# Performance work log

Hardware: AMD Instinct MI355X
Metric: run time of the kernel (lower is better)

Reference implementation:

```python
import jax, jax.numpy as jnp
import numpy as np

N_NODES = 50000
N_EDGES = 800000
IN_DIM = 100
HIDDEN = 16
N_CLASSES = 40


def setup_inputs() -> dict:
    key = jax.random.key(0)
    k1, k2, k3, k4, k5, k6 = jax.random.split(key, 6)
    features = jax.random.normal(k1, (N_NODES, IN_DIM), dtype=jnp.float32)
    edge_src = jax.random.randint(k2, (N_EDGES,), 0, N_NODES, dtype=jnp.int32)
    edge_dst = jax.random.randint(k3, (N_EDGES,), 0, N_NODES, dtype=jnp.int32)
    edge_vals = jax.random.uniform(k4, (N_EDGES,), dtype=jnp.float32)
    W1 = jax.random.uniform(k5, (IN_DIM, HIDDEN), dtype=jnp.float32)
    W2 = jax.random.uniform(k6, (HIDDEN, N_CLASSES), dtype=jnp.float32)
    return {"features": features, "edge_src": edge_src, "edge_dst": edge_dst,
            "edge_vals": edge_vals, "W1": W1, "W2": W2}


def _spmm(edge_src, edge_dst, edge_vals, x):
    # z = A @ x with A given as (dst, src, val) edge list; equivalent to the
    # partition-loop addmm accumulation in broadcast().
    msgs = edge_vals[:, None] * x[edge_src]            # [E, d]
    return jax.ops.segment_sum(msgs, edge_dst, num_segments=x.shape[0])


def reference(features, edge_src, edge_dst, edge_vals, W1, W2):
    h = jax.nn.relu(_spmm(edge_src, edge_dst, edge_vals, features) @ W1)  # [N, 16]
    out = _spmm(edge_src, edge_dst, edge_vals, h) @ W2                    # [N, C]
    return jax.nn.log_softmax(out, axis=1)
```

## Files before the change

kernel.cpp:

```cpp
#include <hip/hip_runtime.h>

#define N_NODES   50000
#define N_EDGES   800000
#define IN_DIM    100
#define HIDDEN    16
#define N_CLASSES 40

#define BSHIFT 6
#define NPB    64
#define NBKT   782
#define PB     256
#define EPB    3125
#define BTW    (NBKT + 1)
#define CAP    2048

#define GROWS 64
__global__ __launch_bounds__(256) void gemm_xw1(const float* __restrict__ X,
                                                const float* __restrict__ W,
                                                float* __restrict__ Y) {
    __shared__ __align__(16) float sX[GROWS * IN_DIM];
    __shared__ __align__(16) float sW[IN_DIM * HIDDEN];
    const int tid  = threadIdx.x;
    const int row0 = blockIdx.x * GROWS;
    const int nrows = min(GROWS, N_NODES - row0);

    const float4* W4 = (const float4*)W;
    float4* sW4 = (float4*)sW;
    for (int i = tid; i < (IN_DIM * HIDDEN) / 4; i += 256) sW4[i] = W4[i];

    const float4* X4 = (const float4*)(X + (size_t)row0 * IN_DIM);
    float4* sX4 = (float4*)sX;
    const int nf4 = nrows * (IN_DIM / 4);
    for (int i = tid; i < nf4; i += 256) sX4[i] = X4[i];
    __syncthreads();

    const int r = tid >> 2;
    const int q = tid & 3;
    if (r >= nrows) return;

    float4 acc = make_float4(0.f, 0.f, 0.f, 0.f);
    const float* xr = &sX[r * IN_DIM];
#pragma unroll
    for (int k = 0; k < IN_DIM; ++k) {
        const float xk = xr[k];
        const float4 w = *(const float4*)&sW[k * HIDDEN + q * 4];
        acc.x = fmaf(xk, w.x, acc.x);
        acc.y = fmaf(xk, w.y, acc.y);
        acc.z = fmaf(xk, w.z, acc.z);
        acc.w = fmaf(xk, w.w, acc.w);
    }
    *(float4*)&Y[(size_t)(row0 + r) * HIDDEN + q * 4] = acc;
}

__global__ __launch_bounds__(512) void partition_kernel(const int* __restrict__ src,
                                                        const int* __restrict__ dst,
                                                        const float* __restrict__ val,
                                                        int* __restrict__ BT,
                                                        int2* __restrict__ binned) {
    __shared__ int  cnt[NBKT];
    __shared__ int  lcur[NBKT];
    __shared__ int  sd[512];
    __shared__ int2 staged[EPB];

    const int tid = threadIdx.x, b = blockIdx.x;
    const int e0 = b * EPB;

    for (int k = tid; k < NBKT; k += 512) cnt[k] = 0;
    __syncthreads();
    for (int i = tid; i < EPB; i += 512)
        atomicAdd(&cnt[dst[e0 + i] >> BSHIFT], 1);
    __syncthreads();

    const int k0 = 2 * tid, k1 = 2 * tid + 1;
    const int a  = (k0 < NBKT) ? cnt[k0] : 0;
    const int bb = (k1 < NBKT) ? cnt[k1] : 0;
    const int s  = a + bb;
    sd[tid] = s;
    __syncthreads();
    for (int off = 1; off < 512; off <<= 1) {
        const int u = (tid >= off) ? sd[tid - off] : 0;
        __syncthreads();
        sd[tid] += u;
        __syncthreads();
    }
    const int excl = sd[tid] - s;
    if (k0 < NBKT) { lcur[k0] = excl;     BT[b * BTW + k0] = excl; }
    if (k1 < NBKT) { lcur[k1] = excl + a; BT[b * BTW + k1] = excl + a; }
    if (tid == 0)  BT[b * BTW + NBKT] = EPB;
    __syncthreads();

    for (int i = tid; i < EPB; i += 512) {
        const int e = e0 + i;
        const int d = dst[e];
        const int k = d >> BSHIFT;
        const int pos = atomicAdd(&lcur[k], 1);
        staged[pos] = make_int2(src[e] | ((d & (NPB - 1)) << 16),
                                __float_as_int(val[e]));
    }
    __syncthreads();

    for (int i = tid; i < EPB; i += 512)
        binned[e0 + i] = staged[i];
}

__global__ __launch_bounds__(256) void sort_kernel(const int* __restrict__ BT,
                                                   const int2* __restrict__ binned,
                                                   int2* __restrict__ sorted,
                                                   int2* __restrict__ meta) {
    __shared__ int  cnt[NPB];
    __shared__ int  cur[NPB];
    __shared__ int  sTot;
    __shared__ int2 staged[CAP];

    const int tid = threadIdx.x, k = blockIdx.x;
    if (tid < NPB) cnt[tid] = 0;
    __syncthreads();

    const int rs = BT[tid * BTW + k];
    const int re = BT[tid * BTW + k + 1];
    const int2* rb = binned + (size_t)tid * EPB;

    for (int p = rs; p < re; ++p)
        atomicAdd(&cnt[(rb[p].x >> 16) & (NPB - 1)], 1);
    __syncthreads();

    if (tid < NPB) {
        const int v = cnt[tid];
        int x = v;
#pragma unroll
        for (int d = 1; d < 64; d <<= 1) {
            const int y = __shfl_up(x, d, 64);
            if (tid >= d) x += y;
        }
        const int excl = x - v;
        cur[tid] = excl;
        const int node = k * NPB + tid;
        if (node < N_NODES) meta[node] = make_int2(k * CAP + excl, v);
        if (tid == NPB - 1) sTot = x;
    }
    __syncthreads();

    for (int p = rs; p < re; ++p) {
        const int2 e = rb[p];
        const int  n = (e.x >> 16) & (NPB - 1);
        const int pos = atomicAdd(&cur[n], 1);
        staged[pos] = make_int2(e.x & 0xFFFF, e.y);
    }
    __syncthreads();

    const int m = sTot;
    for (int i = tid; i < m; i += 256)
        sorted[(size_t)k * CAP + i] = staged[i];
}

__global__ __launch_bounds__(256) void gather_relu(const int2* __restrict__ meta,
                                                   const int2* __restrict__ sorted,
                                                   const float* __restrict__ X,
                                                   float* __restrict__ Z) {
    const int tid = threadIdx.x;
    const int n = blockIdx.x * 16 + (tid >> 4);
    const int j = tid & 15;
    const int2 md = meta[n];
    const int beg = md.x, end = md.x + md.y;

    float acc = 0.f;
    int p = beg;
    for (; p + 4 <= end; p += 4) {
        const int2 e0 = sorted[p];
        const int2 e1 = sorted[p + 1];
        const int2 e2 = sorted[p + 2];
        const int2 e3 = sorted[p + 3];
        const float x0 = X[(size_t)e0.x * HIDDEN + j];
        const float x1 = X[(size_t)e1.x * HIDDEN + j];
        const float x2 = X[(size_t)e2.x * HIDDEN + j];
        const float x3 = X[(size_t)e3.x * HIDDEN + j];
        acc = fmaf(__int_as_float(e0.y), x0, acc);
        acc = fmaf(__int_as_float(e1.y), x1, acc);
        acc = fmaf(__int_as_float(e2.y), x2, acc);
        acc = fmaf(__int_as_float(e3.y), x3, acc);
    }
    for (; p < end; ++p) {
        const int2 e = sorted[p];
        acc = fmaf(__int_as_float(e.y), X[(size_t)e.x * HIDDEN + j], acc);
    }
    Z[(size_t)n * HIDDEN + j] = fmaxf(acc, 0.f);
}

__global__ __launch_bounds__(256) void gather_out(const int2* __restrict__ meta,
                                                  const int2* __restrict__ sorted,
                                                  const float* __restrict__ X,
                                                  const float* __restrict__ W2,
                                                  float* __restrict__ out) {
    __shared__ float sW[688];
    __shared__ float zt[16 * HIDDEN];
    const int tid = threadIdx.x;
    for (int i = tid; i < HIDDEN * N_CLASSES; i += 256) sW[i] = W2[i];

    const int g = tid >> 4;
    const int j = tid & 15;
    const int n = blockIdx.x * 16 + g;

    const int2 md = meta[n];
    const int beg = md.x, end = md.x + md.y;
    float acc = 0.f;
    int p = beg;
    for (; p + 4 <= end; p += 4) {
        const int2 e0 = sorted[p];
        const int2 e1 = sorted[p + 1];
        const int2 e2 = sorted[p + 2];
        const int2 e3 = sorted[p + 3];
        const float x0 = X[(size_t)e0.x * HIDDEN + j];
        const float x1 = X[(size_t)e1.x * HIDDEN + j];
        const float x2 = X[(size_t)e2.x * HIDDEN + j];
        const float x3 = X[(size_t)e3.x * HIDDEN + j];
        acc = fmaf(__int_as_float(e0.y), x0, acc);
        acc = fmaf(__int_as_float(e1.y), x1, acc);
        acc = fmaf(__int_as_float(e2.y), x2, acc);
        acc = fmaf(__int_as_float(e3.y), x3, acc);
    }
    for (; p < end; ++p) {
        const int2 e = sorted[p];
        acc = fmaf(__int_as_float(e.y), X[(size_t)e.x * HIDDEN + j], acc);
    }
    zt[g * HIDDEN + j] = acc;
    __syncthreads();

    float o0 = 0.f, o1 = 0.f, o2 = 0.f;
    const float* zr = &zt[g * HIDDEN];
#pragma unroll
    for (int k = 0; k < HIDDEN; ++k) {
        const float zk = zr[k];
        o0 = fmaf(zk, sW[k * N_CLASSES + j], o0);
        o1 = fmaf(zk, sW[k * N_CLASSES + j + 16], o1);
        o2 = fmaf(zk, sW[k * N_CLASSES + j + 32], o2);
    }
    const bool has3 = (j < 8);
    float m = fmaxf(o0, o1);
    if (has3) m = fmaxf(m, o2);
#pragma unroll
    for (int d = 1; d < 16; d <<= 1) m = fmaxf(m, __shfl_xor(m, d, 16));
    float se = __expf(o0 - m) + __expf(o1 - m);
    if (has3) se += __expf(o2 - m);
#pragma unroll
    for (int d = 1; d < 16; d <<= 1) se += __shfl_xor(se, d, 16);
    const float lse = m + __logf(se);

    float* orow = out + (size_t)n * N_CLASSES;
    orow[j]      = o0 - lse;
    orow[j + 16] = o1 - lse;
    if (has3) orow[j + 32] = o2 - lse;
}

extern "C" void kernel_launch(void* const* d_in, const int* in_sizes, int n_in,
                              void* d_out, int out_size, void* d_ws, size_t ws_size,
                              hipStream_t stream) {
    const float* features = (const float*)d_in[0];
    const int*   edge_src = (const int*)d_in[1];
    const int*   edge_dst = (const int*)d_in[2];
    const float* edge_val = (const float*)d_in[3];
    const float* W1       = (const float*)d_in[4];
    const float* W2       = (const float*)d_in[5];
    float*       out      = (float*)d_out;

    char* base = (char*)d_ws;
    const size_t HNB = (size_t)N_NODES * HIDDEN * sizeof(float);
    float* y1     = (float*)(base);
    float* z1     = (float*)(base + HNB);
    int2*  binned = (int2*) (base + 2 * HNB);
    int2*  sortd  = (int2*) (base + 2 * HNB + (size_t)N_EDGES * 8);
    char*  tail   = base + 2 * HNB + (size_t)N_EDGES * 8
                         + (size_t)NBKT * CAP * 8;
    int*   BT     = (int*) (tail);
    int2*  meta   = (int2*)(tail + ((size_t)PB * BTW * 4 + 255 & ~255ULL));

    partition_kernel<<<PB, 512, 0, stream>>>(edge_src, edge_dst, edge_val, BT, binned);
    sort_kernel<<<NBKT, 256, 0, stream>>>(BT, binned, sortd, meta);

    gemm_xw1<<<(N_NODES + GROWS - 1) / GROWS, 256, 0, stream>>>(features, W1, y1);
    gather_relu<<<N_NODES / 16, 256, 0, stream>>>(meta, sortd, y1, z1);
    gather_out<<<N_NODES / 16, 256, 0, stream>>>(meta, sortd, z1, W2, out);
}
```

Before: 140.9 us.

## Transpose bucket table, vectorize SpMM gathers with float2 and paired edge loads

Stores the per-partition bucket offsets transposed so sort_kernel's per-thread reads are coalesced. Pads each node's edge segment to even length so edges can be loaded as int4 pairs, and rewrites both gather kernels to use 8 threads per node loading float2 features, with 32 nodes per block. The output kernel computes 5 classes per thread with a padded shared tile. This adds extra padding inside sorted buckets and slightly more register use per thread.

```diff
diff --git a/kernel.cpp b/kernel.cpp
--- a/kernel.cpp
+++ b/kernel.cpp
@@ -11,8 +11,8 @@
 #define NBKT   782
 #define PB     256
 #define EPB    3125
-#define BTW    (NBKT + 1)
 #define CAP    2048
+#define GNODES 32
 
 #define GROWS 64
 __global__ __launch_bounds__(256) void gemm_xw1(const float* __restrict__ X,
@@ -55,7 +55,7 @@
 __global__ __launch_bounds__(512) void partition_kernel(const int* __restrict__ src,
                                                         const int* __restrict__ dst,
                                                         const float* __restrict__ val,
-                                                        int* __restrict__ BT,
+                                                        int* __restrict__ BTt,
                                                         int2* __restrict__ binned) {
     __shared__ int  cnt[NBKT];
     __shared__ int  lcur[NBKT];
@@ -84,9 +84,9 @@
         __syncthreads();
     }
     const int excl = sd[tid] - s;
-    if (k0 < NBKT) { lcur[k0] = excl;     BT[b * BTW + k0] = excl; }
-    if (k1 < NBKT) { lcur[k1] = excl + a; BT[b * BTW + k1] = excl + a; }
-    if (tid == 0)  BT[b * BTW + NBKT] = EPB;
+    if (k0 < NBKT) { lcur[k0] = excl;     BTt[k0 * PB + b] = excl; }
+    if (k1 < NBKT) { lcur[k1] = excl + a; BTt[k1 * PB + b] = excl + a; }
+    if (tid == 0)  BTt[NBKT * PB + b] = EPB;
     __syncthreads();
 
     for (int i = tid; i < EPB; i += 512) {
@@ -103,7 +103,7 @@
         binned[e0 + i] = staged[i];
 }
 
-__global__ __launch_bounds__(256) void sort_kernel(const int* __restrict__ BT,
+__global__ __launch_bounds__(256) void sort_kernel(const int* __restrict__ BTt,
                                                    const int2* __restrict__ binned,
                                                    int2* __restrict__ sorted,
                                                    int2* __restrict__ meta) {
@@ -116,8 +116,8 @@
     if (tid < NPB) cnt[tid] = 0;
     __syncthreads();
 
-    const int rs = BT[tid * BTW + k];
-    const int re = BT[tid * BTW + k + 1];
+    const int rs = BTt[k * PB + tid];
+    const int re = BTt[(k + 1) * PB + tid];
     const int2* rb = binned + (size_t)tid * EPB;
 
     for (int p = rs; p < re; ++p)
@@ -125,14 +125,15 @@
     __syncthreads();
 
     if (tid < NPB) {
-        const int v = cnt[tid];
-        int x = v;
+        const int v  = cnt[tid];
+        const int vp = (v + 1) & ~1;
+        int x = vp;
 #pragma unroll
         for (int d = 1; d < 64; d <<= 1) {
             const int y = __shfl_up(x, d, 64);
             if (tid >= d) x += y;
         }
-        const int excl = x - v;
+        const int excl = x - vp;
         cur[tid] = excl;
         const int node = k * NPB + tid;
         if (node < N_NODES) meta[node] = make_int2(k * CAP + excl, v);
@@ -153,37 +154,43 @@
         sorted[(size_t)k * CAP + i] = staged[i];
 }
 
-__global__ __launch_bounds__(256) void gather_relu(const int2* __restrict__ meta,
+template <bool RELU_OUT>
+__global__ __launch_bounds__(256) void gather_spmm(const int2* __restrict__ meta,
                                                    const int2* __restrict__ sorted,
                                                    const float* __restrict__ X,
                                                    float* __restrict__ Z) {
     const int tid = threadIdx.x;
-    const int n = blockIdx.x * 16 + (tid >> 4);
-    const int j = tid & 15;
+    const int g = tid >> 3, j = tid & 7;
+    const int n = blockIdx.x * GNODES + g;
+    if (n >= N_NODES) return;
     const int2 md = meta[n];
     const int beg = md.x, end = md.x + md.y;
-
-    float acc = 0.f;
+    const float2* X2 = (const float2*)X;
+
+    float2 acc = make_float2(0.f, 0.f);
     int p = beg;
     for (; p + 4 <= end; p += 4) {
-        const int2 e0 = sorted[p];
-        const int2 e1 = sorted[p + 1];
-        const int2 e2 = sorted[p + 2];
-        const int2 e3 = sorted[p + 3];
-        const float x0 = X[(size_t)e0.x * HIDDEN + j];
-        const float x1 = X[(size_t)e1.x * HIDDEN + j];
-        const float x2 = X[(size_t)e2.x * HIDDEN + j];
-        const float x3 = X[(size_t)e3.x * HIDDEN + j];
-        acc = fmaf(__int_as_float(e0.y), x0, acc);
-        acc = fmaf(__int_as_float(e1.y), x1, acc);
-        acc = fmaf(__int_as_float(e2.y), x2, acc);
-        acc = fmaf(__int_as_float(e3.y), x3, acc);
+        const int4 ea = *(const int4*)&sorted[p];
+        const int4 eb = *(const int4*)&sorted[p + 2];
+        const float2 x0 = X2[(size_t)ea.x * 8 + j];
+        const float2 x1 = X2[(size_t)ea.z * 8 + j];
+        const float2 x2 = X2[(size_t)eb.x * 8 + j];
+        const float2 x3 = X2[(size_t)eb.z * 8 + j];
+        const float v0 = __int_as_float(ea.y), v1 = __int_as_float(ea.w);
+        const float v2 = __int_as_float(eb.y), v3 = __int_as_float(eb.w);
+        acc.x = fmaf(v0, x0.x, acc.x); acc.y = fmaf(v0, x0.y, acc.y);
+        acc.x = fmaf(v1, x1.x, acc.x); acc.y = fmaf(v1, x1.y, acc.y);
+        acc.x = fmaf(v2, x2.x, acc.x); acc.y = fmaf(v2, x2.y, acc.y);
+        acc.x = fmaf(v3, x3.x, acc.x); acc.y = fmaf(v3, x3.y, acc.y);
     }
     for (; p < end; ++p) {
         const int2 e = sorted[p];
-        acc = fmaf(__int_as_float(e.y), X[(size_t)e.x * HIDDEN + j], acc);
-    }
-    Z[(size_t)n * HIDDEN + j] = fmaxf(acc, 0.f);
+        const float2 x = X2[(size_t)e.x * 8 + j];
+        const float v = __int_as_float(e.y);
+        acc.x = fmaf(v, x.x, acc.x); acc.y = fmaf(v, x.y, acc.y);
+    }
+    if (RELU_OUT) { acc.x = fmaxf(acc.x, 0.f); acc.y = fmaxf(acc.y, 0.f); }
+    ((float2*)Z)[(size_t)n * 8 + j] = acc;
 }
 
 __global__ __launch_bounds__(256) void gather_out(const int2* __restrict__ meta,
@@ -191,64 +198,76 @@
                                                   const float* __restrict__ X,
                                                   const float* __restrict__ W2,
                                                   float* __restrict__ out) {
-    __shared__ float sW[688];
-    __shared__ float zt[16 * HIDDEN];
+    __shared__ float sW[HIDDEN * N_CLASSES];
+    __shared__ float zt[GNODES * 17];
     const int tid = threadIdx.x;
     for (int i = tid; i < HIDDEN * N_CLASSES; i += 256) sW[i] = W2[i];
 
-    const int g = tid >> 4;
-    const int j = tid & 15;
-    const int n = blockIdx.x * 16 + g;
-
-    const int2 md = meta[n];
-    const int beg = md.x, end = md.x + md.y;
-    float acc = 0.f;
-    int p = beg;
-    for (; p + 4 <= end; p += 4) {
-        const int2 e0 = sorted[p];
-        const int2 e1 = sorted[p + 1];
-        const int2 e2 = sorted[p + 2];
-        const int2 e3 = sorted[p + 3];
-        const float x0 = X[(size_t)e0.x * HIDDEN + j];
-        const float x1 = X[(size_t)e1.x * HIDDEN + j];
-        const float x2 = X[(size_t)e2.x * HIDDEN + j];
-        const float x3 = X[(size_t)e3.x * HIDDEN + j];
-        acc = fmaf(__int_as_float(e0.y), x0, acc);
-        acc = fmaf(__int_as_float(e1.y), x1, acc);
-        acc = fmaf(__int_as_float(e2.y), x2, acc);
-        acc = fmaf(__int_as_float(e3.y), x3, acc);
-    }
-    for (; p < end; ++p) {
-        const int2 e = sorted[p];
-        acc = fmaf(__int_as_float(e.y), X[(size_t)e.x * HIDDEN + j], acc);
-    }
-    zt[g * HIDDEN + j] = acc;
-    __syncthreads();
-
-    float o0 = 0.f, o1 = 0.f, o2 = 0.f;
-    const float* zr = &zt[g * HIDDEN];
+    const int g = tid >> 3, j = tid & 7;
+    const int n = blockIdx.x * GNODES + g;
+
+    float2 acc = make_float2(0.f, 0.f);
+    if (n < N_NODES) {
+        const int2 md = meta[n];
+        const int beg = md.x, end = md.x + md.y;
+        const float2* X2 = (const float2*)X;
+        int p = beg;
+        for (; p + 4 <= end; p += 4) {
+            const int4 ea = *(const int4*)&sorted[p];
+            const int4 eb = *(const int4*)&sorted[p + 2];
+            const float2 x0 = X2[(size_t)ea.x * 8 + j];
+            const float2 x1 = X2[(size_t)ea.z * 8 + j];
+            const float2 x2 = X2[(size_t)eb.x * 8 + j];
+            const float2 x3 = X2[(size_t)eb.z * 8 + j];
+            const float v0 = __int_as_float(ea.y), v1 = __int_as_float(ea.w);
+            const float v2 = __int_as_float(eb.y), v3 = __int_as_float(eb.w);
+            acc.x = fmaf(v0, x0.x, acc.x); acc.y = fmaf(v0, x0.y, acc.y);
+            acc.x = fmaf(v1, x1.x, acc.x); acc.y = fmaf(v1, x1.y, acc.y);
+            acc.x = fmaf(v2, x2.x, acc.x); acc.y = fmaf(v2, x2.y, acc.y);
+            acc.x = fmaf(v3, x3.x, acc.x); acc.y = fmaf(v3, x3.y, acc.y);
+        }
+        for (; p < end; ++p) {
+            const int2 e = sorted[p];
+            const float2 x = X2[(size_t)e.x * 8 + j];
+            const float v = __int_as_float(e.y);
+            acc.x = fmaf(v, x.x, acc.x); acc.y = fmaf(v, x.y, acc.y);
+        }
+    }
+    zt[g * 17 + j * 2]     = acc.x;
+    zt[g * 17 + j * 2 + 1] = acc.y;
+    __syncthreads();
+    if (n >= N_NODES) return;
+
+    float z[HIDDEN];
+#pragma unroll
+    for (int k = 0; k < HIDDEN; ++k) z[k] = zt[g * 17 + k];
+
+    float o[5];
+#pragma unroll
+    for (int i = 0; i < 5; ++i) o[i] = 0.f;
 #pragma unroll
     for (int k = 0; k < HIDDEN; ++k) {
-        const float zk = zr[k];
-        o0 = fmaf(zk, sW[k * N_CLASSES + j], o0);
-        o1 = fmaf(zk, sW[k * N_CLASSES + j + 16], o1);
-        o2 = fmaf(zk, sW[k * N_CLASSES + j + 32], o2);
-    }
-    const bool has3 = (j < 8);
-    float m = fmaxf(o0, o1);
-    if (has3) m = fmaxf(m, o2);
-#pragma unroll
-    for (int d = 1; d < 16; d <<= 1) m = fmaxf(m, __shfl_xor(m, d, 16));
-    float se = __expf(o0 - m) + __expf(o1 - m);
-    if (has3) se += __expf(o2 - m);
-#pragma unroll
-    for (int d = 1; d < 16; d <<= 1) se += __shfl_xor(se, d, 16);
+        const float zk = z[k];
+#pragma unroll
+        for (int i = 0; i < 5; ++i)
+            o[i] = fmaf(zk, sW[k * N_CLASSES + j * 5 + i], o[i]);
+    }
+
+    float m = o[0];
+#pragma unroll
+    for (int i = 1; i < 5; ++i) m = fmaxf(m, o[i]);
+#pragma unroll
+    for (int d = 1; d < 8; d <<= 1) m = fmaxf(m, __shfl_xor(m, d, 8));
+    float se = 0.f;
+#pragma unroll
+    for (int i = 0; i < 5; ++i) se += __expf(o[i] - m);
+#pragma unroll
+    for (int d = 1; d < 8; d <<= 1) se += __shfl_xor(se, d, 8);
     const float lse = m + __logf(se);
 
-    float* orow = out + (size_t)n * N_CLASSES;
-    orow[j]      = o0 - lse;
-    orow[j + 16] = o1 - lse;
-    if (has3) orow[j + 32] = o2 - lse;
+    float* orow = out + (size_t)n * N_CLASSES + j * 5;
+#pragma unroll
+    for (int i = 0; i < 5; ++i) orow[i] = o[i] - lse;
 }
 
 extern "C" void kernel_launch(void* const* d_in, const int* in_sizes, int n_in,
@@ -270,13 +289,13 @@
     int2*  sortd  = (int2*) (base + 2 * HNB + (size_t)N_EDGES * 8);
     char*  tail   = base + 2 * HNB + (size_t)N_EDGES * 8
                          + (size_t)NBKT * CAP * 8;
-    int*   BT     = (int*) (tail);
-    int2*  meta   = (int2*)(tail + ((size_t)PB * BTW * 4 + 255 & ~255ULL));
-
-    partition_kernel<<<PB, 512, 0, stream>>>(edge_src, edge_dst, edge_val, BT, binned);
-    sort_kernel<<<NBKT, 256, 0, stream>>>(BT, binned, sortd, meta);
+    int*   BTt    = (int*) (tail);
+    int2*  meta   = (int2*)(tail + (((size_t)(NBKT + 1) * PB * 4 + 255) & ~255ULL));
+
+    partition_kernel<<<PB, 512, 0, stream>>>(edge_src, edge_dst, edge_val, BTt, binned);
+    sort_kernel<<<NBKT, 256, 0, stream>>>(BTt, binned, sortd, meta);
 
     gemm_xw1<<<(N_NODES + GROWS - 1) / GROWS, 256, 0, stream>>>(features, W1, y1);
-    gather_relu<<<N_NODES / 16, 256, 0, stream>>>(meta, sortd, y1, z1);
-    gather_out<<<N_NODES / 16, 256, 0, stream>>>(meta, sortd, z1, W2, out);
-}
+    gather_spmm<true><<<(N_NODES + GNODES - 1) / GNODES, 256, 0, stream>>>(meta, sortd, y1, z1);
+    gather_out<<<(N_NODES + GNODES - 1) / GNODES, 256, 0, stream>>>(meta, sortd, z1, W2, out);
+}
```

Result: no change. 139.1 us (-1.3%).
